# Kernel optimization log

Hardware: AMD Instinct MI355X
Metric: run time of the kernel (lower is better)

The kernel has to match this reference:

```python
import jax, jax.numpy as jnp
import numpy as np

V, E, H, Ld, NL = 32000, 256, 512, 512, 2   # vocab, embed, enc hidden, latent (=dec hidden), layers
S, T = 1024, 512                            # encoder src len, decoder target len


def setup_inputs() -> dict:
    key = jax.random.key(0)
    ks = jax.random.split(key, 20)
    n = lambda k, shp: jax.random.normal(k, shp, dtype=jnp.float32) * 0.05
    return {
        "x": jax.random.randint(ks[0], (S,), 0, V),
        "y": jax.random.randint(ks[1], (T,), 0, V),
        "emb": n(ks[2], (V, E)),
        # encoder LSTM (input E -> hidden H, 2 layers); bias = b_ih + b_hh combined
        "enc_Wih0": n(ks[3], (4 * H, E)), "enc_Whh0": n(ks[4], (4 * H, H)), "enc_b0": n(ks[5], (4 * H,)),
        "enc_Wih1": n(ks[6], (4 * H, H)), "enc_Whh1": n(ks[7], (4 * H, H)), "enc_b1": n(ks[8], (4 * H,)),
        "enc_fcW": n(ks[9], (Ld, H)), "enc_fcb": n(ks[10], (Ld,)),
        # decoder LSTM: input size is 1 (token id as float!), hidden Ld, 2 layers
        "dec_Wih0": n(ks[11], (4 * Ld, 1)), "dec_Whh0": n(ks[12], (4 * Ld, Ld)), "dec_b0": n(ks[13], (4 * Ld,)),
        "dec_Wih1": n(ks[14], (4 * Ld, Ld)), "dec_Whh1": n(ks[15], (4 * Ld, Ld)), "dec_b1": n(ks[16], (4 * Ld,)),
        "dec_fcW": n(ks[17], (V, Ld)), "dec_fcb": n(ks[18], (V,)),
    }


def _cell(x_in, h, c, Wih, Whh, b):
    # torch LSTM gate order: i, f, g, o
    g = Wih @ x_in + Whh @ h + b
    i, f, gg, o = jnp.split(g, 4)
    c2 = jax.nn.sigmoid(f) * c + jax.nn.sigmoid(i) * jnp.tanh(gg)
    h2 = jax.nn.sigmoid(o) * jnp.tanh(c2)
    return h2, c2


def reference(x, y, emb,
              enc_Wih0, enc_Whh0, enc_b0, enc_Wih1, enc_Whh1, enc_b1,
              enc_fcW, enc_fcb,
              dec_Wih0, dec_Whh0, dec_b0, dec_Wih1, dec_Whh1, dec_b1,
              dec_fcW, dec_fcb):
    encW = [(enc_Wih0, enc_Whh0, enc_b0), (enc_Wih1, enc_Whh1, enc_b1)]
    decW = [(dec_Wih0, dec_Whh0, dec_b0), (dec_Wih1, dec_Whh1, dec_b1)]

    # ---- Encoder: embed + 2-layer LSTM over the source, keep final h ----
    em = emb[x]  # [S, E]

    def enc_step(carry, e_t):
        h, c = carry  # each [NL, H]
        inp = e_t
        hs, cs = [], []
        for l in range(NL):
            Wih, Whh, b = encW[l]
            hl, cl = _cell(inp, h[l], c[l], Wih, Whh, b)
            hs.append(hl); cs.append(cl)
            inp = hl
        return (jnp.stack(hs), jnp.stack(cs)), None

    init = (jnp.zeros((NL, H), jnp.float32), jnp.zeros((NL, H), jnp.float32))
    (h_enc, _), _ = jax.lax.scan(enc_step, init, em)

    z = jax.nn.relu(enc_fcW @ h_enc[-1] + enc_fcb)        # [Ld]
    h0 = jnp.tile(z[None, :], (NL, 1))                    # torch.cat([fc]*num_layers)
    c0 = h0                                               # h_c_enc = h_s_initial in source

    def dec_step(carry, _):
        tok, h, c = carry  # tok: scalar float token id, h/c: [NL, Ld]
        inp = tok[None]    # x.reshape(-1,1).to(float32) with one token -> input dim 1
        hs, cs = [], []
        for l in range(NL):
            Wih, Whh, b = decW[l]
            hl, cl = _cell(inp, h[l], c[l], Wih, Whh, b)
            hs.append(hl); cs.append(cl)
            inp = hl
        logits = dec_fcW @ hs[-1] + dec_fcb               # [V]
        nxt = jnp.argmax(logits).astype(jnp.float32)      # best_guess
        return (nxt, jnp.stack(hs), jnp.stack(cs)), logits

    tok0 = y[0].astype(jnp.float32)
    _, logits_seq = jax.lax.scan(dec_step, (tok0, h0, c0), None, length=T - 1)  # [T-1, V]

    # outputs[0] stays zeros, as in the source (loop starts at i=1); training mode -> raw logits
    return jnp.concatenate([jnp.zeros((1, V), jnp.float32), logits_seq], axis=0)
```

## Files before the change

### kernel.cpp

```cpp
#include <hip/hip_runtime.h>
#include <cmath>

#define NWG 256
#define NTHR 1024

static constexpr int kV = 32000;
static constexpr int kS = 1024;
static constexpr int kT = 512;

static constexpr int kLdsRows = 61;

static constexpr int kOffH0  = kLdsRows * 512;
static constexpr int kOffH1  = kOffH0 + 512;
static constexpr int kOffG   = kOffH1 + 512;
static constexpr int kOffPK  = kOffG + 16;
static constexpr int kOffTok = kOffPK + 32;
static constexpr int kOffB   = kOffTok + 1;
static constexpr int kSmemFloats = kOffB + kLdsRows;
static constexpr unsigned kSmemBytes = ((kSmemFloats * 4 + 255) / 256) * 256;

struct SeqParams {
  const int* x; const int* y;
  const float* emb;
  const float* eWih0; const float* eWhh0; const float* eb0;
  const float* eWih1; const float* eWhh1; const float* eb1;
  const float* efcW;  const float* efcb;
  const float* dWih0; const float* dWhh0; const float* db0;
  const float* dWih1; const float* dWhh1; const float* db1;
  const float* dfcW;  const float* dfcb;
  float* out;
  float* P0;
  unsigned long long* h0e;
  unsigned long long* h1e;
  unsigned long long* h0dB;
  unsigned long long* h1dB;
  unsigned long long* candB;
  unsigned* arrive;
  unsigned* go;
  int decApp;
};

__device__ __forceinline__ float sigmf(float v) { return 1.0f / (1.0f + expf(-v)); }

__device__ __forceinline__ float g_ld(const float* p_) {
  return __hip_atomic_load(p_, __ATOMIC_RELAXED, __HIP_MEMORY_SCOPE_AGENT);
}
__device__ __forceinline__ void g_st(float* p_, float v) {
  __hip_atomic_store(p_, v, __ATOMIC_RELAXED, __HIP_MEMORY_SCOPE_AGENT);
}
__device__ __forceinline__ unsigned long long g_ld64(const unsigned long long* p_) {
  return __hip_atomic_load(p_, __ATOMIC_RELAXED, __HIP_MEMORY_SCOPE_AGENT);
}
__device__ __forceinline__ void g_st64(unsigned long long* p_, unsigned long long v) {
  __hip_atomic_store(p_, v, __ATOMIC_RELAXED, __HIP_MEMORY_SCOPE_AGENT);
}

__device__ __forceinline__ float dot4(float4 a, float4 b) {
  return a.x * b.x + a.y * b.y + a.z * b.z + a.w * b.w;
}
__device__ __forceinline__ float wred(float a) {
  a += __shfl_down(a, 32);
  a += __shfl_down(a, 16);
  a += __shfl_down(a, 8);
  a += __shfl_down(a, 4);
  a += __shfl_down(a, 2);
  a += __shfl_down(a, 1);
  return a;
}
__device__ __forceinline__ int swzg(int g) { return g ^ ((g >> 3) & 7); }

__device__ __forceinline__ void pub_write(unsigned long long* pub, int idx,
                                          unsigned tag, float v) {
  g_st64(&pub[idx],
         ((unsigned long long)tag << 32) | (unsigned long long)__float_as_uint(v));
}

template <int SLP>
__device__ __forceinline__ void poll_stage(const unsigned long long* pub,
                                           unsigned tag, float* dst,
                                           int wave8, int lane) {
  const int idx = (wave8 << 6) | lane;
  unsigned long long x;
  for (;;) {
    x = g_ld64(&pub[idx]);
    if (__all((unsigned)(x >> 32) == tag)) break;
    __builtin_amdgcn_s_sleep(SLP);
  }
  dst[idx] = __uint_as_float((unsigned)x);
}

template <int SLP>
__device__ __forceinline__ unsigned long long resolve64(
    unsigned long long x, const unsigned long long* pub, unsigned tag,
    int idx) {
  while (!__all((unsigned)(x >> 32) == tag)) {
    __builtin_amdgcn_s_sleep(SLP);
    x = g_ld64(&pub[idx]);
  }
  return x;
}

__device__ __forceinline__ unsigned long long* hrow(unsigned long long* b,
                                                    int app, int s) {
  return b + (size_t)(app ? s : (s & 1)) * 512;
}
__device__ __forceinline__ unsigned long long* crow(unsigned long long* b,
                                                    int app, int t) {
  return b + (app ? (size_t)t * 256 : 0);
}

__device__ void grid_barrier(const SeqParams& p, unsigned gen) {
  __syncthreads();
  const int tid = threadIdx.x;
  if (blockIdx.x == 0) {
    if (tid > 0 && tid < 256) {
      while (__hip_atomic_load(&p.arrive[tid * 32], __ATOMIC_RELAXED,
                               __HIP_MEMORY_SCOPE_AGENT) < gen)
        __builtin_amdgcn_s_sleep(1);
    }
    __syncthreads();
    if (tid > 0 && tid < 256) {
      __hip_atomic_store(&p.go[tid * 32], gen, __ATOMIC_RELAXED,
                         __HIP_MEMORY_SCOPE_AGENT);
    }
  } else {
    if (tid == 0) {
      __hip_atomic_store(&p.arrive[blockIdx.x * 32], gen, __ATOMIC_RELAXED,
                         __HIP_MEMORY_SCOPE_AGENT);
      while (__hip_atomic_load(&p.go[blockIdx.x * 32], __ATOMIC_RELAXED,
                               __HIP_MEMORY_SCOPE_AGENT) < gen)
        __builtin_amdgcn_s_sleep(1);
    }
    __syncthreads();
  }
}

__device__ __forceinline__ unsigned long long pack_cand(float a, int row,
                                                        unsigned tag) {
  const unsigned u = __float_as_uint(a);
  const unsigned key = u ^ (unsigned)(((int)u >> 31) | 0x80000000);
  return ((unsigned long long)key << 32) |
         ((unsigned long long)(0x7FFFu ^ (unsigned)row) << 17) |
         (unsigned long long)tag;
}

__global__ __launch_bounds__(NTHR, 4) void seq2seq_kernel(SeqParams p) {
  extern __shared__ float smem[];
  float* lds_w  = smem;
  float* lds_h0 = smem + kOffH0;
  float* lds_h1 = smem + kOffH1;
  float* lds_g  = smem + kOffG;
  unsigned long long* lds_pk =
      reinterpret_cast<unsigned long long*>(smem + kOffPK);
  float* lds_tok = smem + kOffTok;
  float* lds_b   = smem + kOffB;

  const int w = blockIdx.x;
  const int tid = threadIdx.x;
  const int wave = tid >> 6, lane = tid & 63;
  const int app = p.decApp;

  {
    float* lds_em = lds_w;
    const int t0  = (w & 127) * 8;
    const int row = (w >> 7) * 1024 + tid;
    float4* emv = reinterpret_cast<float4*>(lds_em);
    if (tid < 512) {
      const int tl = tid >> 6, kq = tid & 63;
      const int tk = p.x[t0 + tl];
      emv[tid] = reinterpret_cast<const float4*>(p.emb)[(size_t)tk * 64 + kq];
    }
    __syncthreads();
    float acc[8];
    const float b = p.eb0[row];
#pragma unroll
    for (int t = 0; t < 8; ++t) acc[t] = b;
    for (int kc = 0; kc < 4; ++kc) {
      float4 wv[16];
      const float4* wr =
          reinterpret_cast<const float4*>(p.eWih0 + (size_t)row * 256) + kc * 16;
#pragma unroll
      for (int i = 0; i < 16; ++i) wv[i] = wr[i];
#pragma unroll
      for (int t = 0; t < 8; ++t) {
        const float4* ev =
            reinterpret_cast<const float4*>(lds_em + t * 256) + kc * 16;
        float a = acc[t];
#pragma unroll
        for (int i = 0; i < 16; ++i) a += dot4(wv[i], ev[i]);
        acc[t] = a;
      }
    }
#pragma unroll
    for (int t = 0; t < 8; ++t)
      g_st(&p.P0[(size_t)(t0 + t) * 2048 + row], acc[t]);
    if (tid < 4) {
      if (w < 128) pub_write(p.h0e, w * 4 + tid, 1u, 0.f);
      else         pub_write(p.h1e, (w - 128) * 4 + tid, 1u, 0.f);
    }
    __syncthreads();

    const float4* gw4 =
        reinterpret_cast<const float4*>(p.dfcW + (size_t)w * 125 * 512);
    float4* lw4 = reinterpret_cast<float4*>(lds_w);
    for (int i = tid; i < kLdsRows * 128; i += NTHR)
      lw4[(i & ~127) | ((i & 127) ^ ((i >> 3) & 7))] = gw4[i];
    if (tid < kLdsRows) lds_b[tid] = p.dfcb[w * 125 + tid];
  }
  grid_barrier(p, 1u);

  if (w < 128) {
    const int row_l0 = (wave & 3) * 512 + w * 4 + (wave >> 2);
    float pv_next = 0.f;
    if (lane == 0) pv_next = g_ld(&p.P0[row_l0]);
    float c0e = 0.f;
    for (int i = 0; i < kS; ++i) {
      if (wave < 8)
        poll_stage<2>(p.h0e + (size_t)i * 512, (unsigned)(i + 1), lds_h0,
                      wave, lane);
      __syncthreads();
      const float pv = pv_next;
      if (lane == 0 && i + 1 < kS)
        pv_next = g_ld(&p.P0[(size_t)(i + 1) * 2048 + row_l0]);
      const float4* W4 =
          reinterpret_cast<const float4*>(p.eWhh0 + (size_t)row_l0 * 512);
      const float4* h4 = reinterpret_cast<const float4*>(lds_h0);
      float a = dot4(W4[lane * 2], h4[lane * 2]) +
                dot4(W4[lane * 2 + 1], h4[lane * 2 + 1]);
      a = wred(a);
      if (lane == 0) lds_g[wave] = a + pv;
      __syncthreads();
      if (tid < 4) {
        const float gi = lds_g[tid * 4 + 0];
        const float gf = lds_g[tid * 4 + 1];
        const float gg = lds_g[tid * 4 + 2];
        const float go = lds_g[tid * 4 + 3];
        const float c2 = sigmf(gf) * c0e + sigmf(gi) * tanhf(gg);
        c0e = c2;
        pub_write(p.h0e, (int)((size_t)(i + 1) * 512) + w * 4 + tid,
                  (unsigned)(i + 2), sigmf(go) * tanhf(c2));
      }
    }
  } else {
    const int ww = w - 128;
    const int row = (wave & 3) * 512 + ww * 4 + (wave >> 2);
    float c1e = 0.f;
    for (int j = 0; j < kS; ++j) {
      if (wave < 8)
        poll_stage<2>(p.h0e + (size_t)(j + 1) * 512, (unsigned)(j + 2),
                      lds_h0, wave, lane);
      else
        poll_stage<2>(p.h1e + (size_t)j * 512, (unsigned)(j + 1), lds_h1,
                      wave - 8, lane);
      __syncthreads();
      const float4* Wa =
          reinterpret_cast<const float4*>(p.eWih1 + (size_t)row * 512);
      const float4* Wb =
          reinterpret_cast<const float4*>(p.eWhh1 + (size_t)row * 512);
      const float4* h4a = reinterpret_cast<const float4*>(lds_h0);
      const float4* h4b = reinterpret_cast<const float4*>(lds_h1);
      float a = (lane == 0) ? p.eb1[row] : 0.f;
      a += dot4(Wa[lane * 2], h4a[lane * 2]) +
           dot4(Wa[lane * 2 + 1], h4a[lane * 2 + 1]);
      a += dot4(Wb[lane * 2], h4b[lane * 2]) +
           dot4(Wb[lane * 2 + 1], h4b[lane * 2 + 1]);
      a = wred(a);
      if (lane == 0) lds_g[wave] = a;
      __syncthreads();
      if (tid < 4) {
        const float gi = lds_g[tid * 4 + 0];
        const float gf = lds_g[tid * 4 + 1];
        const float gg = lds_g[tid * 4 + 2];
        const float go = lds_g[tid * 4 + 3];
        const float c2 = sigmf(gf) * c1e + sigmf(gi) * tanhf(gg);
        c1e = c2;
        pub_write(p.h1e, (int)((size_t)(j + 1) * 512) + ww * 4 + tid,
                  (unsigned)(j + 2), sigmf(go) * tanhf(c2));
      }
    }
  }

  float c0d = 0.f, c1d = 0.f;
  {
    if (wave < 8)
      poll_stage<2>(p.h1e + (size_t)kS * 512, (unsigned)(kS + 1), lds_h0,
                    wave, lane);
    __syncthreads();
    if (wave < 2) {
      const int u = w * 2 + wave;
      const float4* W4 =
          reinterpret_cast<const float4*>(p.efcW + (size_t)u * 512);
      const float4* h4 = reinterpret_cast<const float4*>(lds_h0);
      float a = dot4(W4[lane * 2], h4[lane * 2]) +
                dot4(W4[lane * 2 + 1], h4[lane * 2 + 1]);
      a = wred(a);
      if (lane == 0) lds_g[wave] = fmaxf(a + p.efcb[u], 0.f);
    }
    __syncthreads();
    if (tid < 2) {
      const int uu = w * 2 + tid;
      const float z = lds_g[tid];
      c0d = z; c1d = z;
      pub_write(hrow(p.h0dB, app, 0), uu, 1u, z);
      pub_write(hrow(p.h1dB, app, 0), uu, 1u, z);
    }
  }

  float4 Ra0, Rb0, Ra1, Rb1, Ra2, Rb2, Ra3, Rb3;
  float bi0, bi1, bi2, bi3;
  {
    const int rb = w * 125 + kLdsRows + wave * 4;
#define LWR(i)                                                                \
  {                                                                           \
    const float4* q =                                                         \
        reinterpret_cast<const float4*>(p.dfcW + (size_t)(rb + i) * 512) +    \
        lane * 2;                                                             \
    Ra##i = q[0];                                                             \
    Rb##i = q[1];                                                             \
    bi##i = p.dfcb[rb + i];                                                   \
  }
    LWR(0) LWR(1) LWR(2) LWR(3)
#undef LWR
  }
  grid_barrier(p, 2u);

  const int idx = (wave << 6) | lane;
  unsigned long long xB = 0;
  for (int t = 0; t < kT - 1; ++t) {
    {
      if (wave < 8) {
        if (t == 0)
          poll_stage<2>(hrow(p.h0dB, app, 0), 1u, lds_h0, wave, lane);
        else
          lds_h0[idx] = __uint_as_float((unsigned)xB);
      } else if (wave == 15) {
        if (t == 0) {
          if (lane == 0) lds_tok[0] = (float)p.y[0];
        } else {
          const unsigned tagexp = (unsigned)t;
          const unsigned long long* cb = crow(p.candB, app, t);
          unsigned long long k0, k1, k2, k3;
          for (;;) {
            k0 = g_ld64(&cb[lane]);
            k1 = g_ld64(&cb[lane + 64]);
            k2 = g_ld64(&cb[lane + 128]);
            k3 = g_ld64(&cb[lane + 192]);
            const bool ok = ((unsigned)(k0 & 0x1FFFF) == tagexp) &
                            ((unsigned)(k1 & 0x1FFFF) == tagexp) &
                            ((unsigned)(k2 & 0x1FFFF) == tagexp) &
                            ((unsigned)(k3 & 0x1FFFF) == tagexp);
            if (__all(ok)) break;
            __builtin_amdgcn_s_sleep(1);
          }
          unsigned long long pk = k0;
          if (k1 > pk) pk = k1;
          if (k2 > pk) pk = k2;
          if (k3 > pk) pk = k3;
#pragma unroll
          for (int off = 32; off >= 1; off >>= 1) {
            const unsigned long long o = __shfl_down(pk, off);
            if (o > pk) pk = o;
          }
          if (lane == 0)
            lds_tok[0] = (float)(0x7FFFu ^ (unsigned)((pk >> 17) & 0x7FFF));
        }
      }
      __syncthreads();
      if (wave < 8) {
        const int row = (wave & 3) * 512 + w * 2 + (wave >> 2);
        const float4* W4 =
            reinterpret_cast<const float4*>(p.dWhh0 + (size_t)row * 512);
        const float4* h4 = reinterpret_cast<const float4*>(lds_h0);
        float a = dot4(W4[lane * 2], h4[lane * 2]) +
                  dot4(W4[lane * 2 + 1], h4[lane * 2 + 1]);
        a = wred(a);
        if (lane == 0) lds_g[wave] = a;
      }
      __syncthreads();
      if (tid < 2) {
        const float tok = lds_tok[0];
        const int uu = w * 2 + tid;
        float gv[4];
#pragma unroll
        for (int g = 0; g < 4; ++g) {
          const int rg = g * 512 + uu;
          gv[g] = lds_g[tid * 4 + g] + p.dWih0[rg] * tok + p.db0[rg];
        }
        const float c2 = sigmf(gv[1]) * c0d + sigmf(gv[0]) * tanhf(gv[2]);
        c0d = c2;
        pub_write(hrow(p.h0dB, app, t + 1), uu, (unsigned)(t + 2),
                  sigmf(gv[3]) * tanhf(c2));
      }
    }
    {
      if (wave < 8) {
        xB = resolve64<2>(g_ld64(&hrow(p.h0dB, app, t + 1)[idx]),
                          hrow(p.h0dB, app, t + 1), (unsigned)(t + 2), idx);
        lds_h0[idx] = __uint_as_float((unsigned)xB);
      } else {
        poll_stage<2>(hrow(p.h1dB, app, t), (unsigned)(t + 1), lds_h1,
                      wave - 8, lane);
      }
      __syncthreads();
      if (wave < 8) {
        const int row = (wave & 3) * 512 + w * 2 + (wave >> 2);
        const float4* Wa =
            reinterpret_cast<const float4*>(p.dWih1 + (size_t)row * 512);
        const float4* Wb =
            reinterpret_cast<const float4*>(p.dWhh1 + (size_t)row * 512);
        const float4* h4a = reinterpret_cast<const float4*>(lds_h0);
        const float4* h4b = reinterpret_cast<const float4*>(lds_h1);
        float a = (lane == 0) ? p.db1[row] : 0.f;
        a += dot4(Wa[lane * 2], h4a[lane * 2]) +
             dot4(Wa[lane * 2 + 1], h4a[lane * 2 + 1]);
        a += dot4(Wb[lane * 2], h4b[lane * 2]) +
             dot4(Wb[lane * 2 + 1], h4b[lane * 2 + 1]);
        a = wred(a);
        if (lane == 0) lds_g[wave] = a;
      }
      __syncthreads();
      if (tid < 2) {
        const int uu = w * 2 + tid;
        const float gi = lds_g[tid * 4 + 0];
        const float gf = lds_g[tid * 4 + 1];
        const float gg = lds_g[tid * 4 + 2];
        const float go = lds_g[tid * 4 + 3];
        const float c2 = sigmf(gf) * c1d + sigmf(gi) * tanhf(gg);
        c1d = c2;
        pub_write(hrow(p.h1dB, app, t + 1), uu, (unsigned)(t + 2),
                  sigmf(go) * tanhf(c2));
      }
    }
    {
      if (wave < 8)
        poll_stage<2>(hrow(p.h1dB, app, t + 1), (unsigned)(t + 2), lds_h0,
                      wave, lane);
      __syncthreads();
      const float4* h4 = reinterpret_cast<const float4*>(lds_h0);
      const float4 ha = h4[lane * 2], hb = h4[lane * 2 + 1];
      float* orow = p.out + (size_t)(t + 1) * kV;
      const unsigned tagout = (unsigned)(t + 1);
      unsigned long long best = 0;
      const int rb = w * 125 + kLdsRows + wave * 4;
#define FCR(i)                                                                \
  {                                                                           \
    const int row = rb + i;                                                   \
    float a = (lane == 0) ? bi##i : 0.f;                                      \
    a += dot4(Ra##i, ha) + dot4(Rb##i, hb);                                   \
    a = wred(a);                                                              \
    if (lane == 0) {                                                          \
      orow[row] = a;                                                          \
      const unsigned long long pk2 = pack_cand(a, row, tagout);               \
      if (pk2 > best) best = pk2;                                             \
    }                                                                         \
  }
      FCR(0) FCR(1) FCR(2) FCR(3)
#undef FCR
      const float4* lw4 = reinterpret_cast<const float4*>(lds_w);
      for (int rr = wave; rr < kLdsRows; rr += 16) {
        const int row = w * 125 + rr;
        const float4* lwr = lw4 + rr * 128;
        float a = (lane == 0) ? lds_b[rr] : 0.f;
        a += dot4(lwr[swzg(lane * 2)], ha) + dot4(lwr[swzg(lane * 2 + 1)], hb);
        a = wred(a);
        if (lane == 0) {
          orow[row] = a;
          const unsigned long long pk2 = pack_cand(a, row, tagout);
          if (pk2 > best) best = pk2;
        }
      }
      if (lane == 0) lds_pk[wave] = best;
      __syncthreads();
      if (tid == 0) {
        unsigned long long b2 = lds_pk[0];
#pragma unroll
        for (int k2 = 1; k2 < 16; ++k2)
          if (lds_pk[k2] > b2) b2 = lds_pk[k2];
        g_st64(&crow(p.candB, app, (int)tagout)[w], b2);
      }
    }
  }

  {
    const int oidx = w * NTHR + tid;
    if (oidx < kV) p.out[oidx] = 0.f;
  }
}

extern "C" void kernel_launch(void* const* d_in, const int* in_sizes, int n_in,
                              void* d_out, int out_size, void* d_ws, size_t ws_size,
                              hipStream_t stream) {
  (void)in_sizes; (void)n_in; (void)out_size;
  SeqParams P;
  P.x     = (const int*)d_in[0];
  P.y     = (const int*)d_in[1];
  P.emb   = (const float*)d_in[2];
  P.eWih0 = (const float*)d_in[3];
  P.eWhh0 = (const float*)d_in[4];
  P.eb0   = (const float*)d_in[5];
  P.eWih1 = (const float*)d_in[6];
  P.eWhh1 = (const float*)d_in[7];
  P.eb1   = (const float*)d_in[8];
  P.efcW  = (const float*)d_in[9];
  P.efcb  = (const float*)d_in[10];
  P.dWih0 = (const float*)d_in[11];
  P.dWhh0 = (const float*)d_in[12];
  P.db0   = (const float*)d_in[13];
  P.dWih1 = (const float*)d_in[14];
  P.dWhh1 = (const float*)d_in[15];
  P.db1   = (const float*)d_in[16];
  P.dfcW  = (const float*)d_in[17];
  P.dfcb  = (const float*)d_in[18];
  P.out   = (float*)d_out;

  char* ws = (char*)d_ws;
  P.arrive = (unsigned*)ws;
  P.go     = (unsigned*)(ws + 32768);
  unsigned long long* ringC = (unsigned long long*)(ws + 65536);
  unsigned long long* ring0 = (unsigned long long*)(ws + 67584);
  unsigned long long* ring1 = (unsigned long long*)(ws + 75776);

  const size_t dAppO   = 131072ull;
  const size_t kHdB    = 512ull * 512ull * 8ull;
  const size_t kCdB    = 512ull * 256ull * 8ull;
  const size_t dAppEnd = dAppO + 2 * kHdB + kCdB;
  if (ws_size >= dAppEnd) {
    P.h0dB  = (unsigned long long*)(ws + dAppO);
    P.h1dB  = (unsigned long long*)(ws + dAppO + kHdB);
    P.candB = (unsigned long long*)(ws + dAppO + 2 * kHdB);
    P.decApp = 1;
  } else {
    P.h0dB = ring0; P.h1dB = ring1; P.candB = ringC;
    P.decApp = 0;
  }

  const size_t kP0B = 8388608ull;
  const size_t kEpB = 4198400ull;
  const size_t encO = (dAppEnd + 65535ull) & ~65535ull;
  if (ws_size >= encO + kP0B + 2 * kEpB) {
    P.P0  = (float*)(ws + encO);
    P.h0e = (unsigned long long*)(ws + encO + kP0B);
    P.h1e = (unsigned long long*)(ws + encO + kP0B + kEpB);
  } else {
    char* ob = (char*)d_out;
    P.P0  = (float*)ob;
    P.h0e = (unsigned long long*)(ob + kP0B);
    P.h1e = (unsigned long long*)(ob + kP0B + kEpB);
  }

  (void)hipFuncSetAttribute(reinterpret_cast<const void*>(seq2seq_kernel),
                            hipFuncAttributeMaxDynamicSharedMemorySize,
                            (int)kSmemBytes);

  (void)hipMemsetAsync(d_ws, 0, 83968, stream);

  void* args[] = { &P };
  (void)hipLaunchCooperativeKernel(reinterpret_cast<void*>(seq2seq_kernel),
                                   dim3(NWG), dim3(NTHR), args, kSmemBytes,
                                   stream);
}
```

Before: 5.496 ms.

## Run encoder recurrence per-wave with register-resident weights and direct global polling

The encoder LSTM loops are restructured so that each of the first four waves in a workgroup owns one hidden unit and computes all four of its gates. The recurrent weights are held in registers for the whole sequence. Each wave polls the tagged hidden-state buffer straight from global memory into registers, with no LDS staging and no __syncthreads, which removes two block barriers and the LDS round trip from every time step. The trade-offs are higher register pressure, more redundant global polling traffic across waves, and 12 of the 16 waves sitting idle.

```diff
diff --git a/kernel.cpp b/kernel.cpp
--- a/kernel.cpp
+++ b/kernel.cpp
@@ -210,72 +210,129 @@
   grid_barrier(p, 1u);
 
   if (w < 128) {
-    const int row_l0 = (wave & 3) * 512 + w * 4 + (wave >> 2);
-    float pv_next = 0.f;
-    if (lane == 0) pv_next = g_ld(&p.P0[row_l0]);
-    float c0e = 0.f;
-    for (int i = 0; i < kS; ++i) {
-      if (wave < 8)
-        poll_stage<2>(p.h0e + (size_t)i * 512, (unsigned)(i + 1), lds_h0,
-                      wave, lane);
-      __syncthreads();
-      const float pv = pv_next;
-      if (lane == 0 && i + 1 < kS)
-        pv_next = g_ld(&p.P0[(size_t)(i + 1) * 2048 + row_l0]);
-      const float4* W4 =
-          reinterpret_cast<const float4*>(p.eWhh0 + (size_t)row_l0 * 512);
-      const float4* h4 = reinterpret_cast<const float4*>(lds_h0);
-      float a = dot4(W4[lane * 2], h4[lane * 2]) +
-                dot4(W4[lane * 2 + 1], h4[lane * 2 + 1]);
-      a = wred(a);
-      if (lane == 0) lds_g[wave] = a + pv;
-      __syncthreads();
-      if (tid < 4) {
-        const float gi = lds_g[tid * 4 + 0];
-        const float gf = lds_g[tid * 4 + 1];
-        const float gg = lds_g[tid * 4 + 2];
-        const float go = lds_g[tid * 4 + 3];
-        const float c2 = sigmf(gf) * c0e + sigmf(gi) * tanhf(gg);
-        c0e = c2;
-        pub_write(p.h0e, (int)((size_t)(i + 1) * 512) + w * 4 + tid,
-                  (unsigned)(i + 2), sigmf(go) * tanhf(c2));
+    if (wave < 4) {
+      const int u4 = w * 4 + wave;
+      float4 Wk[4][2];
+#pragma unroll
+      for (int g = 0; g < 4; ++g) {
+        const float4* wr = reinterpret_cast<const float4*>(
+            p.eWhh0 + (size_t)(g * 512 + u4) * 512) + lane * 2;
+        Wk[g][0] = wr[0]; Wk[g][1] = wr[1];
+      }
+      float c0e = 0.f;
+      for (int i = 0; i < kS; ++i) {
+        float pv[4];
+        if (lane == 0) {
+#pragma unroll
+          for (int g = 0; g < 4; ++g)
+            pv[g] = g_ld(&p.P0[(size_t)i * 2048 + g * 512 + u4]);
+        }
+        const unsigned long long* hb = p.h0e + (size_t)i * 512 + lane * 8;
+        const unsigned tg = (unsigned)(i + 1);
+        unsigned long long xs[8];
+#pragma unroll
+        for (int k = 0; k < 8; ++k) xs[k] = g_ld64(hb + k);
+        for (;;) {
+          bool ok = true;
+#pragma unroll
+          for (int k = 0; k < 8; ++k) ok &= ((unsigned)(xs[k] >> 32) == tg);
+          if (__all(ok)) break;
+          __builtin_amdgcn_s_sleep(2);
+#pragma unroll
+          for (int k = 0; k < 8; ++k) xs[k] = g_ld64(hb + k);
+        }
+        float4 hA, hB;
+        hA.x = __uint_as_float((unsigned)xs[0]);
+        hA.y = __uint_as_float((unsigned)xs[1]);
+        hA.z = __uint_as_float((unsigned)xs[2]);
+        hA.w = __uint_as_float((unsigned)xs[3]);
+        hB.x = __uint_as_float((unsigned)xs[4]);
+        hB.y = __uint_as_float((unsigned)xs[5]);
+        hB.z = __uint_as_float((unsigned)xs[6]);
+        hB.w = __uint_as_float((unsigned)xs[7]);
+        float gv[4];
+#pragma unroll
+        for (int g = 0; g < 4; ++g)
+          gv[g] = wred(dot4(Wk[g][0], hA) + dot4(Wk[g][1], hB));
+        if (lane == 0) {
+          const float gi = gv[0] + pv[0];
+          const float gf = gv[1] + pv[1];
+          const float gg = gv[2] + pv[2];
+          const float go = gv[3] + pv[3];
+          const float c2 = sigmf(gf) * c0e + sigmf(gi) * tanhf(gg);
+          c0e = c2;
+          pub_write(p.h0e, (int)((size_t)(i + 1) * 512) + u4, tg + 1,
+                    sigmf(go) * tanhf(c2));
+        }
       }
     }
   } else {
-    const int ww = w - 128;
-    const int row = (wave & 3) * 512 + ww * 4 + (wave >> 2);
-    float c1e = 0.f;
-    for (int j = 0; j < kS; ++j) {
-      if (wave < 8)
-        poll_stage<2>(p.h0e + (size_t)(j + 1) * 512, (unsigned)(j + 2),
-                      lds_h0, wave, lane);
-      else
-        poll_stage<2>(p.h1e + (size_t)j * 512, (unsigned)(j + 1), lds_h1,
-                      wave - 8, lane);
-      __syncthreads();
-      const float4* Wa =
-          reinterpret_cast<const float4*>(p.eWih1 + (size_t)row * 512);
-      const float4* Wb =
-          reinterpret_cast<const float4*>(p.eWhh1 + (size_t)row * 512);
-      const float4* h4a = reinterpret_cast<const float4*>(lds_h0);
-      const float4* h4b = reinterpret_cast<const float4*>(lds_h1);
-      float a = (lane == 0) ? p.eb1[row] : 0.f;
-      a += dot4(Wa[lane * 2], h4a[lane * 2]) +
-           dot4(Wa[lane * 2 + 1], h4a[lane * 2 + 1]);
-      a += dot4(Wb[lane * 2], h4b[lane * 2]) +
-           dot4(Wb[lane * 2 + 1], h4b[lane * 2 + 1]);
-      a = wred(a);
-      if (lane == 0) lds_g[wave] = a;
-      __syncthreads();
-      if (tid < 4) {
-        const float gi = lds_g[tid * 4 + 0];
-        const float gf = lds_g[tid * 4 + 1];
-        const float gg = lds_g[tid * 4 + 2];
-        const float go = lds_g[tid * 4 + 3];
-        const float c2 = sigmf(gf) * c1e + sigmf(gi) * tanhf(gg);
-        c1e = c2;
-        pub_write(p.h1e, (int)((size_t)(j + 1) * 512) + ww * 4 + tid,
-                  (unsigned)(j + 2), sigmf(go) * tanhf(c2));
+    if (wave < 4) {
+      const int u4 = (w - 128) * 4 + wave;
+      float4 Ak[4][2], Bk[4][2];
+      float bias[4];
+#pragma unroll
+      for (int g = 0; g < 4; ++g) {
+        const float4* wa = reinterpret_cast<const float4*>(
+            p.eWih1 + (size_t)(g * 512 + u4) * 512) + lane * 2;
+        const float4* wb = reinterpret_cast<const float4*>(
+            p.eWhh1 + (size_t)(g * 512 + u4) * 512) + lane * 2;
+        Ak[g][0] = wa[0]; Ak[g][1] = wa[1];
+        Bk[g][0] = wb[0]; Bk[g][1] = wb[1];
+        bias[g] = p.eb1[g * 512 + u4];
+      }
+      float c1e = 0.f;
+      for (int j = 0; j < kS; ++j) {
+        const unsigned long long* ha_ =
+            p.h0e + (size_t)(j + 1) * 512 + lane * 8;
+        const unsigned long long* hb_ = p.h1e + (size_t)j * 512 + lane * 8;
+        const unsigned ta = (unsigned)(j + 2), tb = (unsigned)(j + 1);
+        unsigned long long xa[8], xb[8];
+#pragma unroll
+        for (int k = 0; k < 8; ++k) { xa[k] = g_ld64(ha_ + k); xb[k] = g_ld64(hb_ + k); }
+        for (;;) {
+          bool ok = true;
+#pragma unroll
+          for (int k = 0; k < 8; ++k) {
+            ok &= ((unsigned)(xa[k] >> 32) == ta);
+            ok &= ((unsigned)(xb[k] >> 32) == tb);
+          }
+          if (__all(ok)) break;
+          __builtin_amdgcn_s_sleep(2);
+#pragma unroll
+          for (int k = 0; k < 8; ++k) { xa[k] = g_ld64(ha_ + k); xb[k] = g_ld64(hb_ + k); }
+        }
+        float4 hA0, hA1, hB0, hB1;
+        hA0.x = __uint_as_float((unsigned)xa[0]);
+        hA0.y = __uint_as_float((unsigned)xa[1]);
+        hA0.z = __uint_as_float((unsigned)xa[2]);
+        hA0.w = __uint_as_float((unsigned)xa[3]);
+        hA1.x = __uint_as_float((unsigned)xa[4]);
+        hA1.y = __uint_as_float((unsigned)xa[5]);
+        hA1.z = __uint_as_float((unsigned)xa[6]);
+        hA1.w = __uint_as_float((unsigned)xa[7]);
+        hB0.x = __uint_as_float((unsigned)xb[0]);
+        hB0.y = __uint_as_float((unsigned)xb[1]);
+        hB0.z = __uint_as_float((unsigned)xb[2]);
+        hB0.w = __uint_as_float((unsigned)xb[3]);
+        hB1.x = __uint_as_float((unsigned)xb[4]);
+        hB1.y = __uint_as_float((unsigned)xb[5]);
+        hB1.z = __uint_as_float((unsigned)xb[6]);
+        hB1.w = __uint_as_float((unsigned)xb[7]);
+        float gv[4];
+#pragma unroll
+        for (int g = 0; g < 4; ++g) {
+          float a = (lane == 0) ? bias[g] : 0.f;
+          a += dot4(Ak[g][0], hA0) + dot4(Ak[g][1], hA1);
+          a += dot4(Bk[g][0], hB0) + dot4(Bk[g][1], hB1);
+          gv[g] = wred(a);
+        }
+        if (lane == 0) {
+          const float c2 = sigmf(gv[1]) * c1e + sigmf(gv[0]) * tanhf(gv[2]);
+          c1e = c2;
+          pub_write(p.h1e, (int)((size_t)(j + 1) * 512) + u4, ta,
+                    sigmf(gv[3]) * tanhf(c2));
+        }
       }
     }
   }
```

New measurement: 8.511 ms. 1.55x slower.
